# Kernel tuning notes

Measured on AMD Instinct MI355X. Metric: run time of the kernel, lower is better.

Reference implementation:

```python
import jax, jax.numpy as jnp
import numpy as np

CODEBOOK_SIZE = 8192
EMBED_DIM = 256


def setup_inputs() -> dict:
    key = jax.random.key(0)
    k1, k2 = jax.random.split(key)
    z = jax.random.normal(k1, (8, 4096, EMBED_DIM), dtype=jnp.float32)
    # matches torch init: uniform_(-1/codebook_size, 1/codebook_size)
    codebook = jax.random.uniform(
        k2, (CODEBOOK_SIZE, EMBED_DIM), dtype=jnp.float32,
        minval=-1.0 / CODEBOOK_SIZE, maxval=1.0 / CODEBOOK_SIZE)
    return {"z": z, "codebook": codebook}


def reference(z, codebook):
    # z: [B, S, D]; codebook: [K, D]
    z_flat = z.reshape(-1, z.shape[-1])                      # [N, D]
    # ||z||^2 - 2 z.E^T + ||E||^2  -> [N, K]
    distances = (
        jnp.sum(z_flat * z_flat, axis=1, keepdims=True)
        - 2.0 * jnp.einsum("nd,kd->nk", z_flat, codebook)
        + jnp.sum(codebook * codebook, axis=1)
    )
    encoding_indices = jnp.argmin(distances, axis=1)         # [N]
    z_q = codebook[encoding_indices].reshape(z.shape)        # [B, S, D]
    return z_q, encoding_indices
```

## Files before the change

### kernel.cpp

```cpp
#include <hip/hip_runtime.h>


#define NROWS 32768
#define DIM   256
#define KCB   8192
#define CANDCAP 128
#define MARGIN  4.5e-4f
#define WBUF    320

#define SB_CAND  0u
#define SB_CNT   8388608u
#define SB_ZSQ   8519680u
#define SB_CSQ   8650752u
#define SB_CSQ1  8683520u
#define SB_OVL   8716288u
#define SB_OVC   8847360u
#define SB_IMG   8847424u
#define SB_NEED  13041728u

using bf16x8 = __attribute__((ext_vector_type(8))) short;
using f32x4  = __attribute__((ext_vector_type(4))) float;
using u32x4  = __attribute__((ext_vector_type(4))) unsigned int;

__device__ __forceinline__ unsigned short bf16rne(float f) {
    unsigned u = __float_as_uint(f);
    unsigned r = u + 0x7FFFu + ((u >> 16) & 1u);
    return (unsigned short)(r >> 16);
}

__device__ __forceinline__ unsigned pack2_bf16(float a, float b) {
    return (unsigned)bf16rne(a) | ((unsigned)bf16rne(b) << 16);
}

__device__ float np_sumsq_256(const float* __restrict__ p) {
#pragma clang fp contract(off)
    float blk[2];
    #pragma unroll
    for (int b = 0; b < 2; ++b) {
        const float4* q4 = reinterpret_cast<const float4*>(p + b * 128);
        float4 a0 = q4[0], a1 = q4[1];
        float r[8];
        r[0] = __fmul_rn(a0.x, a0.x); r[1] = __fmul_rn(a0.y, a0.y);
        r[2] = __fmul_rn(a0.z, a0.z); r[3] = __fmul_rn(a0.w, a0.w);
        r[4] = __fmul_rn(a1.x, a1.x); r[5] = __fmul_rn(a1.y, a1.y);
        r[6] = __fmul_rn(a1.z, a1.z); r[7] = __fmul_rn(a1.w, a1.w);
        #pragma unroll
        for (int i = 2; i < 32; i += 2) {
            a0 = q4[i]; a1 = q4[i + 1];
            r[0] = __fadd_rn(r[0], __fmul_rn(a0.x, a0.x));
            r[1] = __fadd_rn(r[1], __fmul_rn(a0.y, a0.y));
            r[2] = __fadd_rn(r[2], __fmul_rn(a0.z, a0.z));
            r[3] = __fadd_rn(r[3], __fmul_rn(a0.w, a0.w));
            r[4] = __fadd_rn(r[4], __fmul_rn(a1.x, a1.x));
            r[5] = __fadd_rn(r[5], __fmul_rn(a1.y, a1.y));
            r[6] = __fadd_rn(r[6], __fmul_rn(a1.z, a1.z));
            r[7] = __fadd_rn(r[7], __fmul_rn(a1.w, a1.w));
        }
        blk[b] = __fadd_rn(
            __fadd_rn(__fadd_rn(r[0], r[1]), __fadd_rn(r[2], r[3])),
            __fadd_rn(__fadd_rn(r[4], r[5]), __fadd_rn(r[6], r[7])));
    }
    return __fadd_rn(blk[0], blk[1]);
}

__global__ void vq_prep_kernel(const float* __restrict__ z,
                               const float* __restrict__ cb,
                               char* __restrict__ img,
                               float* __restrict__ zsq, float* __restrict__ csq,
                               float* __restrict__ csq1,
                               unsigned* __restrict__ cnt, unsigned* __restrict__ ovc) {
    int t = blockIdx.x * 256 + threadIdx.x;
    if (t < NROWS) cnt[t] = 0;
    if (t == 0) *ovc = 0;
    if (t < 262144) {
        int s = t & 63, kk = (t >> 6) & 7, T = t >> 9;
        int code = s & 15, lhi = s >> 4;
        const float* src = cb + (size_t)(T * 16 + code) * DIM + kk * 32 + lhi * 8;
        float4 v0 = *reinterpret_cast<const float4*>(src);
        float4 v1 = *reinterpret_cast<const float4*>(src + 4);
        uint4 o;
        o.x = pack2_bf16(v0.x, v0.y); o.y = pack2_bf16(v0.z, v0.w);
        o.z = pack2_bf16(v1.x, v1.y); o.w = pack2_bf16(v1.z, v1.w);
        *reinterpret_cast<uint4*>(img + (size_t)T * 8192 + kk * 1024 + s * 16) = o;
    } else if (t < 262144 + KCB) {
        int k = t - 262144;
        float s = np_sumsq_256(cb + (size_t)k * DIM);
        csq[k] = s;
        csq1[k] = s + 1.0f;
    } else if (t < 262144 + KCB + NROWS) {
        int r = t - 262144 - KCB;
        zsq[r] = np_sumsq_256(z + (size_t)r * DIM);
    }
}

__global__ __launch_bounds__(512, 2) void vq_screen_kernel(
    const float* __restrict__ z, const char* __restrict__ img,
    const float* __restrict__ csq1,
    unsigned* __restrict__ cnt, unsigned short* __restrict__ cand) {
    __shared__ unsigned runmin[128];
    __shared__ unsigned wcnt[8];
    __shared__ unsigned wbuf[8][WBUF];
    const int tid = threadIdx.x, lane = tid & 63, wid = tid >> 6;
    const int wr = wid >> 2, wc = wid & 3;
    const int l15 = lane & 15, lhi = lane >> 4;
    const int row0 = blockIdx.x * 128;
    const int tbase = wc * 128;

    bf16x8 ah[4][8];
    #pragma unroll
    for (int m = 0; m < 4; ++m) {
        const float* zr = z + (size_t)(row0 + wr * 64 + m * 16 + l15) * DIM;
        #pragma unroll
        for (int kk = 0; kk < 8; ++kk) {
            float4 v0 = *reinterpret_cast<const float4*>(zr + kk * 32 + lhi * 8);
            float4 v1 = *reinterpret_cast<const float4*>(zr + kk * 32 + lhi * 8 + 4);
            uint4 o;
            o.x = pack2_bf16(v0.x, v0.y); o.y = pack2_bf16(v0.z, v0.w);
            o.z = pack2_bf16(v1.x, v1.y); o.w = pack2_bf16(v1.z, v1.w);
            ah[m][kk] = __builtin_bit_cast(bf16x8, o);
        }
    }

    if (tid < 128) runmin[tid] = 0x7F800000u;
    if (tid < 8) wcnt[tid] = 0;
    __syncthreads();

    f32x4 acc[4];
    #pragma unroll
    for (int m = 0; m < 4; ++m) acc[m] = (f32x4){0.f, 0.f, 0.f, 0.f};

    const char*  gp  = img + (size_t)tbase * 8192 + (size_t)lane * 16;
    const float* cpe = csq1 + tbase * 16 + l15;
    int codeb = tbase * 16 + l15;

    u32x4 bA[8], bB[8], bC[8];

    auto PUSH = [&](int lr, int code) {
        unsigned pi = atomicAdd(&wcnt[wid], 1u);
        if (pi < WBUF) wbuf[wid][pi] = ((unsigned)lr << 13) | (unsigned)code;
        else {
            int grow = row0 + lr;
            unsigned gs = atomicAdd(&cnt[grow], 1u);
            if (gs < CANDCAP) cand[(size_t)grow * CANDCAP + gs] = (unsigned short)code;
        }
    };

#define LOADR(bh)                                                         \
    {                                                                     \
        _Pragma("unroll")                                                 \
        for (int kk = 0; kk < 8; ++kk)                                    \
            bh[kk] = *reinterpret_cast<const u32x4*>(gp + kk * 1024);     \
        gp += 8192;                                                       \
    }

#define MFMAS(bh)                                                         \
    {                                                                     \
        _Pragma("unroll")                                                 \
        for (int kk = 0; kk < 8; ++kk) {                                  \
            bf16x8 bv = __builtin_bit_cast(bf16x8, bh[kk]);               \
            _Pragma("unroll")                                             \
            for (int m = 0; m < 4; ++m)                                   \
                acc[m] = __builtin_amdgcn_mfma_f32_16x16x32_bf16(         \
                    ah[m][kk], bv, acc[m], 0, 0, 0);                      \
        }                                                                 \
    }

#define EPI()                                                             \
    {                                                                     \
        const float csv = *cpe; cpe += 16;                                \
        _Pragma("unroll")                                                 \
        for (int m = 0; m < 4; ++m) {                                     \
            const int lr0 = wr * 64 + m * 16 + lhi * 4;                   \
            uint4 rmb = *reinterpret_cast<const uint4*>(&runmin[lr0]);    \
            float s0 = fmaf(acc[m][0], -2.0f, csv);                       \
            float s1 = fmaf(acc[m][1], -2.0f, csv);                       \
            float s2 = fmaf(acc[m][2], -2.0f, csv);                       \
            float s3 = fmaf(acc[m][3], -2.0f, csv);                       \
            bool c0 = s0 < __uint_as_float(rmb.x) + MARGIN;               \
            bool c1 = s1 < __uint_as_float(rmb.y) + MARGIN;               \
            bool c2 = s2 < __uint_as_float(rmb.z) + MARGIN;               \
            bool c3 = s3 < __uint_as_float(rmb.w) + MARGIN;               \
            if (__any(c0 | c1 | c2 | c3)) {                               \
                if (c0) { if (s0 < __uint_as_float(rmb.x)) atomicMin(&runmin[lr0 + 0], __float_as_uint(s0)); PUSH(lr0 + 0, codeb); } \
                if (c1) { if (s1 < __uint_as_float(rmb.y)) atomicMin(&runmin[lr0 + 1], __float_as_uint(s1)); PUSH(lr0 + 1, codeb); } \
                if (c2) { if (s2 < __uint_as_float(rmb.z)) atomicMin(&runmin[lr0 + 2], __float_as_uint(s2)); PUSH(lr0 + 2, codeb); } \
                if (c3) { if (s3 < __uint_as_float(rmb.w)) atomicMin(&runmin[lr0 + 3], __float_as_uint(s3)); PUSH(lr0 + 3, codeb); } \
            }                                                             \
            acc[m] = (f32x4){0.f, 0.f, 0.f, 0.f};                         \
        }                                                                 \
        codeb += 16;                                                      \
    }

    LOADR(bA);
    LOADR(bB);
    LOADR(bC);
    MFMAS(bA);
    {
        const float csv = *cpe; cpe += 16;
        #pragma unroll
        for (int m = 0; m < 4; ++m) {
            const int lr0 = wr * 64 + m * 16 + lhi * 4;
            #pragma unroll
            for (int r = 0; r < 4; ++r) {
                float s2 = fmaf(acc[m][r], -2.0f, csv);
                float sm = s2;
                sm = fminf(sm, __shfl_xor(sm, 1));
                sm = fminf(sm, __shfl_xor(sm, 2));
                sm = fminf(sm, __shfl_xor(sm, 4));
                sm = fminf(sm, __shfl_xor(sm, 8));
                if (l15 == 0) atomicMin(&runmin[lr0 + r], __float_as_uint(sm));
                if (s2 < sm + MARGIN) PUSH(lr0 + r, codeb);
            }
            acc[m] = (f32x4){0.f, 0.f, 0.f, 0.f};
        }
        codeb += 16;
    }

    for (int g = 0; g < 41; ++g) {
        LOADR(bA);  MFMAS(bB);  EPI();
        LOADR(bB);  MFMAS(bC);  EPI();
        LOADR(bC);  MFMAS(bA);  EPI();
    }
    LOADR(bA);  MFMAS(bB);  EPI();
    LOADR(bB);  MFMAS(bC);  EPI();
    MFMAS(bA);  EPI();
    MFMAS(bB);  EPI();

    unsigned n = wcnt[wid]; if (n > WBUF) n = WBUF;
    for (unsigned e = lane; e < n; e += 64) {
        unsigned u = wbuf[wid][e];
        int row = row0 + (int)(u >> 13);
        int code = (int)(u & 8191u);
        unsigned slot = atomicAdd(&cnt[row], 1u);
        if (slot < CANDCAP) cand[(size_t)row * CANDCAP + slot] = (unsigned short)code;
    }
#undef LOADR
#undef MFMAS
#undef EPI
}

__global__ __launch_bounds__(256) void vq_exact_kernel(
    const float* __restrict__ z, const float* __restrict__ cb,
    const float* __restrict__ zsq, const float* __restrict__ csq,
    const unsigned* __restrict__ cnt, const unsigned short* __restrict__ cand,
    unsigned* __restrict__ ovl, unsigned* __restrict__ ovc,
    float* __restrict__ idxF, float4* __restrict__ outz, int fused) {
    __shared__ float zrow[4][DIM];
    const int wid = threadIdx.x >> 6, lane = threadIdx.x & 63;
    const int row = blockIdx.x * 4 + wid;

    float4 zv4 = *reinterpret_cast<const float4*>(&z[(size_t)row * DIM + lane * 4]);
    *reinterpret_cast<float4*>(&zrow[wid][lane * 4]) = zv4;
    __syncthreads();

    const unsigned c = cnt[row];
    if (c == 0 || c > CANDCAP) {
        if (lane == 0) { unsigned s = atomicAdd(ovc, 1u); ovl[s] = row; }
        return;
    }

    const float Zr = zsq[row];
    const float4* cb4 = reinterpret_cast<const float4*>(cb);
    float best = 3.4e38f;
    int   bi   = 0x7FFFFFFF;

    for (int j = lane; j < (int)c; j += 64) {
        int k = cand[(size_t)row * CANDCAP + j];
        float a = 0.0f;
        #pragma unroll 8
        for (int q = 0; q < 64; ++q) {
            float4 cv = cb4[(size_t)k * 64 + q];
            float4 zv = *reinterpret_cast<const float4*>(&zrow[wid][q * 4]);
            a = fmaf(zv.x, cv.x, a); a = fmaf(zv.y, cv.y, a);
            a = fmaf(zv.z, cv.z, a); a = fmaf(zv.w, cv.w, a);
        }
        float sv = __fadd_rn(__fsub_rn(Zr, __fmul_rn(2.0f, a)), csq[k]);
        if (sv < best || (sv == best && k < bi)) { best = sv; bi = k; }
    }
    #pragma unroll
    for (int mk = 32; mk >= 1; mk >>= 1) {
        float ov = __shfl_xor(best, mk);
        int   oi = __shfl_xor(bi, mk);
        if (ov < best || (ov == best && oi < bi)) { best = ov; bi = oi; }
    }
    if (lane == 0) idxF[row] = (float)bi;
    if (fused) outz[(size_t)row * 64 + lane] = cb4[(size_t)bi * 64 + lane];
}

__global__ __launch_bounds__(256) void vq_cleanup_kernel(
    const float* __restrict__ z, const float* __restrict__ cb,
    const float* __restrict__ zsq, const float* __restrict__ csq,
    const unsigned* __restrict__ ovl, const unsigned* __restrict__ ovc,
    float* __restrict__ idxF, float4* __restrict__ outz, int fused) {
    __shared__ float zrow[DIM];
    __shared__ float wv[4]; __shared__ int wi[4];
    __shared__ int sbi;
    const int lane = threadIdx.x & 63, wid = threadIdx.x >> 6;
    const unsigned count = *ovc;
    for (unsigned w = blockIdx.x; w < count; w += gridDim.x) {
        const int row = ovl[w];
        __syncthreads();
        *reinterpret_cast<float4*>(&zrow[threadIdx.x * 4 & (DIM - 1)]) =
            *reinterpret_cast<const float4*>(&z[(size_t)row * DIM + (threadIdx.x * 4 & (DIM - 1))]);
        __syncthreads();
        const float Zr = zsq[row];
        const float4* cb4 = reinterpret_cast<const float4*>(cb);
        float best = 3.4e38f; int bi = 0x7FFFFFFF;
        for (int k = threadIdx.x; k < KCB; k += 256) {
            float a = 0.0f;
            #pragma unroll 8
            for (int q = 0; q < 64; ++q) {
                float4 cv = cb4[(size_t)k * 64 + q];
                float4 zv = *reinterpret_cast<const float4*>(&zrow[q * 4]);
                a = fmaf(zv.x, cv.x, a); a = fmaf(zv.y, cv.y, a);
                a = fmaf(zv.z, cv.z, a); a = fmaf(zv.w, cv.w, a);
            }
            float sv = __fadd_rn(__fsub_rn(Zr, __fmul_rn(2.0f, a)), csq[k]);
            if (sv < best || (sv == best && k < bi)) { best = sv; bi = k; }
        }
        #pragma unroll
        for (int mk = 32; mk >= 1; mk >>= 1) {
            float ov = __shfl_xor(best, mk);
            int   oi = __shfl_xor(bi, mk);
            if (ov < best || (ov == best && oi < bi)) { best = ov; bi = oi; }
        }
        if (lane == 0) { wv[wid] = best; wi[wid] = bi; }
        __syncthreads();
        if (threadIdx.x == 0) {
            #pragma unroll
            for (int u = 1; u < 4; ++u)
                if (wv[u] < best || (wv[u] == best && wi[u] < bi)) { best = wv[u]; bi = wi[u]; }
            idxF[row] = (float)bi;
            sbi = bi;
        }
        __syncthreads();
        if (fused && threadIdx.x < 64)
            outz[(size_t)row * 64 + threadIdx.x] = cb4[(size_t)sbi * 64 + threadIdx.x];
    }
}

__global__ void vq_gather_kernel(const float* __restrict__ cb,
                                 const float* __restrict__ idxF,
                                 float4* __restrict__ out4) {
    int g = blockIdx.x * blockDim.x + threadIdx.x;
    const float4* cb4 = reinterpret_cast<const float4*>(cb);
    for (int i = g; i < NROWS * 64; i += gridDim.x * blockDim.x) {
        int row = i >> 6, q = i & 63;
        int idx = (int)idxF[row];
        out4[i] = cb4[(size_t)idx * 64 + q];
    }
}

extern "C" void kernel_launch(void* const* d_in, const int* in_sizes, int n_in,
                              void* d_out, int out_size, void* d_ws, size_t ws_size,
                              hipStream_t stream) {
    const float* z  = (const float*)d_in[0];
    const float* cb = (const float*)d_in[1];
    float* out = (float*)d_out;

    const int fused = (ws_size >= (size_t)SB_NEED) ? 1 : 0;
    char* SB = fused ? (char*)d_ws : (char*)d_out;

    unsigned short* candp = (unsigned short*)(SB + SB_CAND);
    unsigned*       cntp  = (unsigned*)(SB + SB_CNT);
    float*          zsq   = (float*)(SB + SB_ZSQ);
    float*          csq   = (float*)(SB + SB_CSQ);
    float*          csq1  = (float*)(SB + SB_CSQ1);
    unsigned*       ovl   = (unsigned*)(SB + SB_OVL);
    unsigned*       ovc   = (unsigned*)(SB + SB_OVC);
    char*           img   = SB + SB_IMG;
    float*          idxF  = out + 8388608;

    vq_prep_kernel<<<(262144 + KCB + NROWS + 255) / 256, 256, 0, stream>>>(
        z, cb, img, zsq, csq, csq1, cntp, ovc);
    vq_screen_kernel<<<NROWS / 128, 512, 0, stream>>>(z, img, csq1, cntp, candp);
    vq_exact_kernel<<<NROWS / 4, 256, 0, stream>>>(
        z, cb, zsq, csq, cntp, candp, ovl, ovc, idxF, (float4*)out, fused);
    vq_cleanup_kernel<<<64, 256, 0, stream>>>(
        z, cb, zsq, csq, ovl, ovc, idxF, (float4*)out, fused);
    if (!fused)
        vq_gather_kernel<<<2048, 256, 0, stream>>>(cb, idxF, (float4*)out);
}
```

Measured before the change: 300.7 us.

## Compute row norms in exact kernel and switch screen to double-buffered loads

The per-row ||z||^2 computation moves out of the prep kernel and into the exact and cleanup kernels, which already hold the row in shared memory. This drops 32K prep threads and the zsq workspace round trip. The screen kernel's codebook pipeline goes from triple to double buffering, with the csq1 value prefetched together with each tile. This frees registers but shortens the prefetch distance, so load latency may be less well hidden.

```diff
diff --git a/kernel.cpp b/kernel.cpp
--- a/kernel.cpp
+++ b/kernel.cpp
@@ -10,13 +10,12 @@
 
 #define SB_CAND  0u
 #define SB_CNT   8388608u
-#define SB_ZSQ   8519680u
-#define SB_CSQ   8650752u
-#define SB_CSQ1  8683520u
-#define SB_OVL   8716288u
-#define SB_OVC   8847360u
-#define SB_IMG   8847424u
-#define SB_NEED  13041728u
+#define SB_CSQ   8519680u
+#define SB_CSQ1  8552448u
+#define SB_OVL   8585216u
+#define SB_OVC   8716288u
+#define SB_IMG   8716304u
+#define SB_NEED  12910608u
 
 using bf16x8 = __attribute__((ext_vector_type(8))) short;
 using f32x4  = __attribute__((ext_vector_type(4))) float;
@@ -63,11 +62,9 @@
     return __fadd_rn(blk[0], blk[1]);
 }
 
-__global__ void vq_prep_kernel(const float* __restrict__ z,
-                               const float* __restrict__ cb,
+__global__ void vq_prep_kernel(const float* __restrict__ cb,
                                char* __restrict__ img,
-                               float* __restrict__ zsq, float* __restrict__ csq,
-                               float* __restrict__ csq1,
+                               float* __restrict__ csq, float* __restrict__ csq1,
                                unsigned* __restrict__ cnt, unsigned* __restrict__ ovc) {
     int t = blockIdx.x * 256 + threadIdx.x;
     if (t < NROWS) cnt[t] = 0;
@@ -87,9 +84,6 @@
         float s = np_sumsq_256(cb + (size_t)k * DIM);
         csq[k] = s;
         csq1[k] = s + 1.0f;
-    } else if (t < 262144 + KCB + NROWS) {
-        int r = t - 262144 - KCB;
-        zsq[r] = np_sumsq_256(z + (size_t)r * DIM);
     }
 }
 
@@ -129,11 +123,12 @@
     #pragma unroll
     for (int m = 0; m < 4; ++m) acc[m] = (f32x4){0.f, 0.f, 0.f, 0.f};
 
-    const char*  gp  = img + (size_t)tbase * 8192 + (size_t)lane * 16;
-    const float* cpe = csq1 + tbase * 16 + l15;
+    const char*  gp = img + (size_t)tbase * 8192 + (size_t)lane * 16;
+    const float* cp = csq1 + tbase * 16 + l15;
     int codeb = tbase * 16 + l15;
 
-    u32x4 bA[8], bB[8], bC[8];
+    u32x4 bA[8]; float csA;
+    u32x4 bB[8]; float csB;
 
     auto PUSH = [&](int lr, int code) {
         unsigned pi = atomicAdd(&wcnt[wid], 1u);
@@ -145,12 +140,13 @@
         }
     };
 
-#define LOADR(bh)                                                         \
+#define LOADR(bh, cs)                                                     \
     {                                                                     \
         _Pragma("unroll")                                                 \
         for (int kk = 0; kk < 8; ++kk)                                    \
             bh[kk] = *reinterpret_cast<const u32x4*>(gp + kk * 1024);     \
-        gp += 8192;                                                       \
+        cs = *cp;                                                         \
+        gp += 8192; cp += 16;                                             \
     }
 
 #define MFMAS(bh)                                                         \
@@ -165,9 +161,8 @@
         }                                                                 \
     }
 
-#define EPI()                                                             \
+#define EPI(csv)                                                          \
     {                                                                     \
-        const float csv = *cpe; cpe += 16;                                \
         _Pragma("unroll")                                                 \
         for (int m = 0; m < 4; ++m) {                                     \
             const int lr0 = wr * 64 + m * 16 + lhi * 4;                   \
@@ -191,18 +186,16 @@
         codeb += 16;                                                      \
     }
 
-    LOADR(bA);
-    LOADR(bB);
-    LOADR(bC);
+    LOADR(bA, csA);
+    LOADR(bB, csB);
     MFMAS(bA);
     {
-        const float csv = *cpe; cpe += 16;
         #pragma unroll
         for (int m = 0; m < 4; ++m) {
             const int lr0 = wr * 64 + m * 16 + lhi * 4;
             #pragma unroll
             for (int r = 0; r < 4; ++r) {
-                float s2 = fmaf(acc[m][r], -2.0f, csv);
+                float s2 = fmaf(acc[m][r], -2.0f, csA);
                 float sm = s2;
                 sm = fminf(sm, __shfl_xor(sm, 1));
                 sm = fminf(sm, __shfl_xor(sm, 2));
@@ -216,15 +209,11 @@
         codeb += 16;
     }
 
-    for (int g = 0; g < 41; ++g) {
-        LOADR(bA);  MFMAS(bB);  EPI();
-        LOADR(bB);  MFMAS(bC);  EPI();
-        LOADR(bC);  MFMAS(bA);  EPI();
-    }
-    LOADR(bA);  MFMAS(bB);  EPI();
-    LOADR(bB);  MFMAS(bC);  EPI();
-    MFMAS(bA);  EPI();
-    MFMAS(bB);  EPI();
+    for (int t = 1; t < 127; t += 2) {
+        LOADR(bA, csA);  MFMAS(bB);  EPI(csB);
+        LOADR(bB, csB);  MFMAS(bA);  EPI(csA);
+    }
+    MFMAS(bB);  EPI(csB);
 
     unsigned n = wcnt[wid]; if (n > WBUF) n = WBUF;
     for (unsigned e = lane; e < n; e += 64) {
@@ -241,7 +230,7 @@
 
 __global__ __launch_bounds__(256) void vq_exact_kernel(
     const float* __restrict__ z, const float* __restrict__ cb,
-    const float* __restrict__ zsq, const float* __restrict__ csq,
+    const float* __restrict__ csq,
     const unsigned* __restrict__ cnt, const unsigned short* __restrict__ cand,
     unsigned* __restrict__ ovl, unsigned* __restrict__ ovc,
     float* __restrict__ idxF, float4* __restrict__ outz, int fused) {
@@ -259,7 +248,7 @@
         return;
     }
 
-    const float Zr = zsq[row];
+    const float Zr = np_sumsq_256(&zrow[wid][0]);
     const float4* cb4 = reinterpret_cast<const float4*>(cb);
     float best = 3.4e38f;
     int   bi   = 0x7FFFFFFF;
@@ -289,7 +278,7 @@
 
 __global__ __launch_bounds__(256) void vq_cleanup_kernel(
     const float* __restrict__ z, const float* __restrict__ cb,
-    const float* __restrict__ zsq, const float* __restrict__ csq,
+    const float* __restrict__ csq,
     const unsigned* __restrict__ ovl, const unsigned* __restrict__ ovc,
     float* __restrict__ idxF, float4* __restrict__ outz, int fused) {
     __shared__ float zrow[DIM];
@@ -303,7 +292,7 @@
         *reinterpret_cast<float4*>(&zrow[threadIdx.x * 4 & (DIM - 1)]) =
             *reinterpret_cast<const float4*>(&z[(size_t)row * DIM + (threadIdx.x * 4 & (DIM - 1))]);
         __syncthreads();
-        const float Zr = zsq[row];
+        const float Zr = np_sumsq_256(&zrow[0]);
         const float4* cb4 = reinterpret_cast<const float4*>(cb);
         float best = 3.4e38f; int bi = 0x7FFFFFFF;
         for (int k = threadIdx.x; k < KCB; k += 256) {
@@ -363,7 +352,6 @@
 
     unsigned short* candp = (unsigned short*)(SB + SB_CAND);
     unsigned*       cntp  = (unsigned*)(SB + SB_CNT);
-    float*          zsq   = (float*)(SB + SB_ZSQ);
     float*          csq   = (float*)(SB + SB_CSQ);
     float*          csq1  = (float*)(SB + SB_CSQ1);
     unsigned*       ovl   = (unsigned*)(SB + SB_OVL);
@@ -371,13 +359,13 @@
     char*           img   = SB + SB_IMG;
     float*          idxF  = out + 8388608;
 
-    vq_prep_kernel<<<(262144 + KCB + NROWS + 255) / 256, 256, 0, stream>>>(
-        z, cb, img, zsq, csq, csq1, cntp, ovc);
+    vq_prep_kernel<<<(262144 + KCB + 255) / 256, 256, 0, stream>>>(
+        cb, img, csq, csq1, cntp, ovc);
     vq_screen_kernel<<<NROWS / 128, 512, 0, stream>>>(z, img, csq1, cntp, candp);
     vq_exact_kernel<<<NROWS / 4, 256, 0, stream>>>(
-        z, cb, zsq, csq, cntp, candp, ovl, ovc, idxF, (float4*)out, fused);
+        z, cb, csq, cntp, candp, ovl, ovc, idxF, (float4*)out, fused);
     vq_cleanup_kernel<<<64, 256, 0, stream>>>(
-        z, cb, zsq, csq, ovl, ovc, idxF, (float4*)out, fused);
+        z, cb, csq, ovl, ovc, idxF, (float4*)out, fused);
     if (!fused)
         vq_gather_kernel<<<2048, 256, 0, stream>>>(cb, idxF, (float4*)out);
 }
```

Result: faster. 289.6 us, median of 2 (-3.7%).
